# Kernel optimization log

Measured on AMD Instinct MI355X. Metric: run time of the kernel, lower is better.

## Reference

```python
import jax, jax.numpy as jnp
import numpy as np

INPUT_CHANNELS = 1
FIRE_RATE = 0.5
BN_EPS = 1e-5
PAD = 3  # (kernel_size - 1) // 2 for kernel_size=7


def setup_inputs() -> dict:
    key = jax.random.key(0)
    ks = jax.random.split(key, 6)
    B, H, W, C, HID, K = 8, 256, 256, 16, 128, 7
    return {
        "x": jax.random.normal(ks[0], (B, H, W, C), jnp.float32),
        "p0_w": jax.random.normal(ks[1], (K, K, 1, C), jnp.float32) * 0.1,
        "p0_b": jax.random.normal(ks[2], (C,), jnp.float32) * 0.1,
        "fc0_w": jax.random.normal(ks[3], (2 * C, HID), jnp.float32) * (1.0 / np.sqrt(2 * C)),
        "fc0_b": jax.random.normal(ks[4], (HID,), jnp.float32) * 0.1,
        "bn_gamma": jnp.ones((HID,), jnp.float32),
        "bn_beta": jnp.zeros((HID,), jnp.float32),
        "fc1_w": jax.random.normal(ks[5], (HID, C), jnp.float32) * (1.0 / np.sqrt(HID)),
        "steps": 10,
    }


def _depthwise_conv(x, w, b):
    # x: [B,H,W,C], w: [K,K,1,C] depthwise, reflect padding
    xp = jnp.pad(x, ((0, 0), (PAD, PAD), (PAD, PAD), (0, 0)), mode="reflect")
    y = jax.lax.conv_general_dilated(
        xp, w, window_strides=(1, 1), padding="VALID",
        dimension_numbers=("NHWC", "HWIO", "NHWC"),
        feature_group_count=x.shape[-1])
    return y + b


def _step(x, key, p0_w, p0_b, fc0_w, fc0_b, bn_gamma, bn_beta, fc1_w):
    B, H, W, C = x.shape
    # perceive: depthwise conv + identity concat -> [B,H,W,2C]
    y = jnp.concatenate([x, _depthwise_conv(x, p0_w, p0_b)], axis=-1)
    h = y @ fc0_w + fc0_b  # [B,H,W,HID]
    # BatchNorm2d with batch stats over (N, spatial), per hidden channel
    mean = jnp.mean(h, axis=(0, 1, 2), keepdims=True)
    var = jnp.var(h, axis=(0, 1, 2), keepdims=True)
    h = (h - mean) * jax.lax.rsqrt(var + BN_EPS) * bn_gamma + bn_beta
    h = jax.nn.relu(h)
    dx = h @ fc1_w  # [B,H,W,C]
    # stochastic per-cell mask: rand > fire_rate
    mask = (jax.random.uniform(key, (B, H, W, 1)) > FIRE_RATE).astype(dx.dtype)
    x2 = x + dx * mask
    # keep input channels unchanged
    return jnp.concatenate([x[..., :INPUT_CHANNELS], x2[..., INPUT_CHANNELS:]], axis=-1)


def reference(x, p0_w, p0_b, fc0_w, fc0_b, bn_gamma, bn_beta, fc1_w, steps):
    key = jax.random.key(42)
    for s in range(steps):
        x = _step(x, jax.random.fold_in(key, s), p0_w, p0_b, fc0_w, fc0_b,
                  bn_gamma, bn_beta, fc1_w)
    return x
```

## Files before the change

### kernel.cpp

```cpp
#include <hip/hip_runtime.h>
#include <stdint.h>


constexpr int Bn = 8;
constexpr int Hn = 256;
constexpr int Wn = 256;
constexpr int Cn = 16;
constexpr int HIDn = 128;
constexpr int NCELLS = Bn * Hn * Wn;
constexpr int NGRP = 1024;
constexpr int NPAIR = 528;
constexpr int NSTAT = 560;
constexpr int STEPS = 10;

typedef __attribute__((ext_vector_type(8))) short bf16x8;
typedef __attribute__((ext_vector_type(4))) float f32x4;

__host__ __device__ inline uint32_t rotl32(uint32_t v, int r) {
  return (v << r) | (v >> (32 - r));
}

__host__ __device__ inline void tf2x32(uint32_t k0, uint32_t k1,
                                       uint32_t& x0, uint32_t& x1) {
  uint32_t k2 = k0 ^ k1 ^ 0x1BD11BDAu;
  x0 += k0; x1 += k1;
  x0 += x1; x1 = rotl32(x1, 13); x1 ^= x0;
  x0 += x1; x1 = rotl32(x1, 15); x1 ^= x0;
  x0 += x1; x1 = rotl32(x1, 26); x1 ^= x0;
  x0 += x1; x1 = rotl32(x1,  6); x1 ^= x0;
  x0 += k1; x1 += k2 + 1u;
  x0 += x1; x1 = rotl32(x1, 17); x1 ^= x0;
  x0 += x1; x1 = rotl32(x1, 29); x1 ^= x0;
  x0 += x1; x1 = rotl32(x1, 16); x1 ^= x0;
  x0 += x1; x1 = rotl32(x1, 24); x1 ^= x0;
  x0 += k2; x1 += k0 + 2u;
  x0 += x1; x1 = rotl32(x1, 13); x1 ^= x0;
  x0 += x1; x1 = rotl32(x1, 15); x1 ^= x0;
  x0 += x1; x1 = rotl32(x1, 26); x1 ^= x0;
  x0 += x1; x1 = rotl32(x1,  6); x1 ^= x0;
  x0 += k0; x1 += k1 + 3u;
  x0 += x1; x1 = rotl32(x1, 17); x1 ^= x0;
  x0 += x1; x1 = rotl32(x1, 29); x1 ^= x0;
  x0 += x1; x1 = rotl32(x1, 16); x1 ^= x0;
  x0 += x1; x1 = rotl32(x1, 24); x1 ^= x0;
  x0 += k1; x1 += k2 + 4u;
  x0 += x1; x1 = rotl32(x1, 13); x1 ^= x0;
  x0 += x1; x1 = rotl32(x1, 15); x1 ^= x0;
  x0 += x1; x1 = rotl32(x1, 26); x1 ^= x0;
  x0 += x1; x1 = rotl32(x1,  6); x1 ^= x0;
  x0 += k2; x1 += k0 + 5u;
}

__device__ inline float cell_mask(uint32_t fk0, uint32_t fk1, uint32_t ci) {
  uint32_t a = 0u, b2 = ci;
  tf2x32(fk0, fk1, a, b2);
  uint32_t bits = a ^ b2;
  float u = __uint_as_float((bits >> 9) | 0x3f800000u) - 1.0f;
  return (u > 0.5f) ? 1.0f : 0.0f;
}

__device__ inline uint32_t f2bf(float f) {
  uint32_t u = __float_as_uint(f);
  return (u + 0x7fffu + ((u >> 16) & 1u)) >> 16;
}

__global__ __launch_bounds__(256) void nca_prep(const float* __restrict__ fc0w,
                                                const float* __restrict__ fc1w,
                                                uint16_t* __restrict__ w0bf,
                                                uint16_t* __restrict__ w1p) {
  int i = blockIdx.x * 256 + threadIdx.x;
  if (i < 4096) {
    int n = i >> 5, k = i & 31;
    w0bf[i] = (uint16_t)f2bf(fc0w[k * HIDn + n]);
  } else {
    int j = i - 4096;
    int c = j >> 7, kl = j & 127;
    int n = (kl & 7) * 16 + (kl >> 3);
    w1p[j] = (uint16_t)f2bf(fc1w[n * 16 + c]);
  }
}

__global__ __launch_bounds__(256, 4) void nca_convgram(
    const float* __restrict__ x, const float* __restrict__ p0w,
    const float* __restrict__ p0b, uint16_t* __restrict__ ybf,
    float* __restrict__ partials) {
  __shared__ float sW[784];
  __shared__ float sB[16];
  __shared__ __align__(16) short sYT[32 * 256];
  __shared__ float sMom[4 * 32];
  int t = threadIdx.x;
  int lane = t & 63, wid = t >> 6;
  int bid = blockIdx.x;
  int b = bid & 7;
  int rest = bid >> 3;
  int h0 = (rest >> 1) * 4;
  int wbase = (rest & 1) * 128;
  for (int i = t; i < 784; i += 256) sW[i] = p0w[i];
  if (t < 16) sB[t] = p0b[t];
  __syncthreads();

  int wl = t & 127;
  int ch0 = (t >> 7) * 8;
  int w = wbase + wl;
  const float* xb = x + (size_t)b * (Hn * Wn * Cn) + ch0;
  float acc[4][8];
#pragma unroll
  for (int j = 0; j < 4; j++)
#pragma unroll
    for (int c = 0; c < 8; c++) acc[j][c] = 0.0f;

#pragma unroll 1
  for (int r = 0; r < 10; r++) {
    int hi = h0 - 3 + r;
    hi = (hi < 0) ? -hi : ((hi >= Hn) ? (2 * Hn - 2 - hi) : hi);
    const float* xr = xb + (size_t)hi * (Wn * Cn);
#pragma unroll
    for (int dx = 0; dx < 7; dx++) {
      int ww = w + dx - 3;
      ww = (ww < 0) ? -ww : ((ww >= Wn) ? (2 * Wn - 2 - ww) : ww);
      const float4* p = reinterpret_cast<const float4*>(xr + (size_t)ww * Cn);
      float4 v0 = p[0], v1 = p[1];
      float v[8];
      v[0] = v0.x; v[1] = v0.y; v[2] = v0.z; v[3] = v0.w;
      v[4] = v1.x; v[5] = v1.y; v[6] = v1.z; v[7] = v1.w;
#pragma unroll
      for (int j = 0; j < 4; j++) {
        if (r >= j && r <= j + 6) {
          const float* wt = sW + ((r - j) * 7 + dx) * 16 + ch0;
#pragma unroll
          for (int c = 0; c < 8; c++) acc[j][c] += wt[c] * v[c];
        }
      }
    }
  }

  int colc = lane & 15, kg = lane >> 4;
  f32x4 g00 = {0.f, 0.f, 0.f, 0.f}, g01 = g00, g11 = g00, m0 = g00, m1 = g00;
  bf16x8 ones;
#pragma unroll
  for (int e = 0; e < 8; e++) ones[e] = (short)0x3F80;

#pragma unroll
  for (int rr = 0; rr < 2; rr++) {
    if (rr) __syncthreads();
#pragma unroll
    for (int jj = 0; jj < 2; jj++) {
      int j = rr * 2 + jj;
      size_t ci = ((size_t)(b * Hn + h0 + j) * Wn + w);
      int cidx = jj * 128 + wl;
      const float4* pc = reinterpret_cast<const float4*>(
          xb + ((size_t)(h0 + j) * Wn + w) * Cn);
      float4 c0v = pc[0], c1v = pc[1];
      float xcv[8];
      xcv[0] = c0v.x; xcv[1] = c0v.y; xcv[2] = c0v.z; xcv[3] = c0v.w;
      xcv[4] = c1v.x; xcv[5] = c1v.y; xcv[6] = c1v.z; xcv[7] = c1v.w;
      uint32_t pkx[4], pkc[4];
#pragma unroll
      for (int q = 0; q < 4; q++)
        pkx[q] = f2bf(xcv[2 * q]) | (f2bf(xcv[2 * q + 1]) << 16);
#pragma unroll
      for (int q = 0; q < 4; q++)
        pkc[q] = f2bf(acc[j][2 * q] + sB[ch0 + 2 * q]) |
                 (f2bf(acc[j][2 * q + 1] + sB[ch0 + 2 * q + 1]) << 16);
      *reinterpret_cast<uint4*>(ybf + ci * 32 + ch0) =
          make_uint4(pkx[0], pkx[1], pkx[2], pkx[3]);
      *reinterpret_cast<uint4*>(ybf + ci * 32 + 16 + ch0) =
          make_uint4(pkc[0], pkc[1], pkc[2], pkc[3]);
#pragma unroll
      for (int q = 0; q < 4; q++) {
        int cA = ch0 + 2 * q, cB = cA + 1;
        sYT[cA * 256 + (cidx ^ ((cA & 7) << 3))] = (short)(uint16_t)(pkx[q] & 0xffffu);
        sYT[cB * 256 + (cidx ^ ((cB & 7) << 3))] = (short)(uint16_t)(pkx[q] >> 16);
        int cC = 16 + cA, cD = 16 + cB;
        sYT[cC * 256 + (cidx ^ ((cC & 7) << 3))] = (short)(uint16_t)(pkc[q] & 0xffffu);
        sYT[cD * 256 + (cidx ^ ((cD & 7) << 3))] = (short)(uint16_t)(pkc[q] >> 16);
      }
    }
    __syncthreads();
#pragma unroll
    for (int s2 = 0; s2 < 2; s2++) {
      int kbase = wid * 64 + s2 * 32 + kg * 8;
      int chA = colc, chB = 16 + colc;
      bf16x8 f0 = *reinterpret_cast<const bf16x8*>(sYT + chA * 256 + (kbase ^ ((chA & 7) << 3)));
      bf16x8 f1 = *reinterpret_cast<const bf16x8*>(sYT + chB * 256 + (kbase ^ ((chB & 7) << 3)));
      g00 = __builtin_amdgcn_mfma_f32_16x16x32_bf16(f0, f0, g00, 0, 0, 0);
      g01 = __builtin_amdgcn_mfma_f32_16x16x32_bf16(f0, f1, g01, 0, 0, 0);
      g11 = __builtin_amdgcn_mfma_f32_16x16x32_bf16(f1, f1, g11, 0, 0, 0);
      m0  = __builtin_amdgcn_mfma_f32_16x16x32_bf16(f0, ones, m0, 0, 0, 0);
      m1  = __builtin_amdgcn_mfma_f32_16x16x32_bf16(f1, ones, m1, 0, 0, 0);
    }
  }
  if (colc == 0) {
#pragma unroll
    for (int r = 0; r < 4; r++) {
      sMom[wid * 32 + kg * 4 + r] = m0[r];
      sMom[wid * 32 + 16 + kg * 4 + r] = m1[r];
    }
  }
  __syncthreads();
  float* sG = reinterpret_cast<float*>(sYT);
  {
    float* sGw = sG + wid * 1024;
#pragma unroll
    for (int r = 0; r < 4; r++) {
      int rr2 = kg * 4 + r;
      sGw[rr2 * 32 + colc] = g00[r];
      sGw[rr2 * 32 + 16 + colc] = g01[r];
      sGw[(16 + rr2) * 32 + 16 + colc] = g11[r];
    }
  }
  __syncthreads();

  float* outp = partials + (size_t)bid * NSTAT;
  for (int e = t; e < NSTAT; e += 256) {
    float a;
    if (e < NPAIR) {
      int ee = e, i = 0;
      while (ee >= (32 - i)) { ee -= (32 - i); i++; }
      int j = i + ee;
      int gi = i * 32 + j;
      a = sG[gi] + sG[1024 + gi] + sG[2048 + gi] + sG[3072 + gi];
    } else {
      int i = e - NPAIR;
      a = sMom[i] + sMom[32 + i] + sMom[64 + i] + sMom[96 + i];
    }
    outp[e] = a;
  }
}

__global__ __launch_bounds__(256) void nca_reduceA(
    const float* __restrict__ partials, double* __restrict__ sred) {
  __shared__ double red[256];
  int e = blockIdx.x;
  int t = threadIdx.x;
  double acc = 0.0;
  for (int row = t; row < NGRP; row += 256)
    acc += (double)partials[(size_t)row * NSTAT + e];
  red[t] = acc;
  __syncthreads();
  for (int s2 = 128; s2 > 0; s2 >>= 1) {
    if (t < s2) red[t] += red[t + s2];
    __syncthreads();
  }
  if (t == 0) sred[e] = red[0];
}

__global__ __launch_bounds__(128) void nca_reduceB(
    const double* __restrict__ sred, const float* __restrict__ fc0w,
    const float* __restrict__ gamma, const float* __restrict__ beta,
    float* __restrict__ ss) {
  __shared__ double S[NSTAT];
  int t = threadIdx.x;
  for (int i = t; i < NSTAT; i += 128) S[i] = sred[i];
  __syncthreads();
  double wv[32];
#pragma unroll
  for (int k = 0; k < 32; k++) wv[k] = (double)fc0w[k * HIDn + t];
  double mean_g = 0.0, q = 0.0;
  int e = 0;
  for (int i = 0; i < 32; i++) {
    mean_g += wv[i] * S[NPAIR + i];
    q += wv[i] * wv[i] * S[e]; e++;
    for (int j = i + 1; j < 32; j++) { q += 2.0 * wv[i] * wv[j] * S[e]; e++; }
  }
  const double invN = 1.0 / (double)NCELLS;
  mean_g *= invN; q *= invN;
  double var = q - mean_g * mean_g;
  double scale = (double)gamma[t] / sqrt(var + 1e-5);
  ss[2 * t]     = (float)scale;
  ss[2 * t + 1] = (float)((double)beta[t] - mean_g * scale);
}

__global__ __launch_bounds__(256) void nca_update_mfma(
    const float* __restrict__ x, const uint16_t* __restrict__ ybf,
    const uint16_t* __restrict__ w0bf, const uint16_t* __restrict__ w1p,
    const float* __restrict__ ssg, float* __restrict__ xout,
    uint32_t fk0, uint32_t fk1) {
  __shared__ short hbuf[4][16 * 128];
  int t = threadIdx.x;
  int lane = t & 63, wid = t >> 6;
  int col = lane & 15, g = lane >> 4;
  short* hb = hbuf[wid];

  bf16x8 b0[8];
#pragma unroll
  for (int nt = 0; nt < 8; nt++) {
    int n = nt * 16 + col;
    b0[nt] = *reinterpret_cast<const bf16x8*>(w0bf + n * 32 + g * 8);
  }
  bf16x8 b2[4];
#pragma unroll
  for (int kk = 0; kk < 4; kk++)
    b2[kk] = *reinterpret_cast<const bf16x8*>(w1p + col * 128 + kk * 32 + g * 8);
  float sc[8], sh[8];
#pragma unroll
  for (int nt = 0; nt < 8; nt++) {
    float2 v = reinterpret_cast<const float2*>(ssg)[nt * 16 + col];
    sc[nt] = v.x; sh[nt] = v.y;
  }

  uint32_t waveBase = (uint32_t)blockIdx.x * 1024u + (uint32_t)wid * 256u;
  for (int grp = 0; grp < 4; grp++) {
    uint32_t grpBase = waveBase + (uint32_t)grp * 64u;
    float mval = cell_mask(fk0, fk1, grpBase + (uint32_t)lane);
#pragma unroll 1
    for (int tt = 0; tt < 4; tt++) {
      uint32_t tb = grpBase + (uint32_t)tt * 16u;
      bf16x8 a0 = *reinterpret_cast<const bf16x8*>(
          ybf + (size_t)(tb + col) * 32 + g * 8);
      float xv[4];
#pragma unroll
      for (int r = 0; r < 4; r++)
        xv[r] = x[(size_t)(tb + g * 4 + r) * Cn + col];
      f32x4 h[8];
#pragma unroll
      for (int nt = 0; nt < 8; nt++) {
        f32x4 z = {0.f, 0.f, 0.f, 0.f};
        h[nt] = __builtin_amdgcn_mfma_f32_16x16x32_bf16(a0, b0[nt], z, 0, 0, 0);
      }
#pragma unroll
      for (int r = 0; r < 4; r++) {
        int m = g * 4 + r;
        uint32_t u[4];
#pragma unroll
        for (int q = 0; q < 4; q++) {
          float v0 = fmaxf(h[2 * q][r] * sc[2 * q] + sh[2 * q], 0.0f);
          float v1 = fmaxf(h[2 * q + 1][r] * sc[2 * q + 1] + sh[2 * q + 1], 0.0f);
          u[q] = f2bf(v0) | (f2bf(v1) << 16);
        }
        int idx = m * 128 + ((col * 8) ^ ((m & 7) << 3));
        *reinterpret_cast<uint4*>(hb + idx) = make_uint4(u[0], u[1], u[2], u[3]);
      }
      f32x4 dx = {0.f, 0.f, 0.f, 0.f};
#pragma unroll
      for (int kk = 0; kk < 4; kk++) {
        int idx = col * 128 + (((kk * 32) + g * 8) ^ ((col & 7) << 3));
        bf16x8 a2 = *reinterpret_cast<const bf16x8*>(hb + idx);
        dx = __builtin_amdgcn_mfma_f32_16x16x32_bf16(a2, b2[kk], dx, 0, 0, 0);
      }
#pragma unroll
      for (int r = 0; r < 4; r++) {
        int m = g * 4 + r;
        float mk = __shfl(mval, tt * 16 + m);
        float o = xv[r] + dx[r] * mk;
        if (col == 0) o = xv[r];
        xout[(size_t)(tb + m) * Cn + col] = o;
      }
    }
  }
}

extern "C" void kernel_launch(void* const* d_in, const int* in_sizes, int n_in,
                              void* d_out, int out_size, void* d_ws, size_t ws_size,
                              hipStream_t stream) {
  (void)in_sizes; (void)n_in; (void)out_size; (void)ws_size;
  const float* x0    = (const float*)d_in[0];
  const float* p0w   = (const float*)d_in[1];
  const float* p0b   = (const float*)d_in[2];
  const float* fc0w  = (const float*)d_in[3];
  const float* gamma = (const float*)d_in[5];
  const float* beta  = (const float*)d_in[6];
  const float* fc1w  = (const float*)d_in[7];

  size_t off = 0;
  float* ws_x = (float*)((char*)d_ws + off); off += (size_t)NCELLS * Cn * 4;
  uint16_t* ws_ybf = (uint16_t*)((char*)d_ws + off); off += (size_t)NCELLS * 32 * 2;
  float* ws_part = (float*)((char*)d_ws + off); off += (size_t)NGRP * NSTAT * 4;
  double* ws_sred = (double*)((char*)d_ws + off); off += (size_t)NSTAT * 8;
  float* ws_ss = (float*)((char*)d_ws + off); off += (size_t)HIDn * 2 * 4;
  uint16_t* ws_w0bf = (uint16_t*)((char*)d_ws + off); off += 4096 * 2;
  uint16_t* ws_w1p = (uint16_t*)((char*)d_ws + off); off += 2048 * 2;
  float* out = (float*)d_out;

  nca_prep<<<24, 256, 0, stream>>>(fc0w, fc1w, ws_w0bf, ws_w1p);

  const float* xin = x0;
  for (int s = 0; s < STEPS; s++) {
    uint32_t fk0 = 0u, fk1 = (uint32_t)s;
    tf2x32(0u, 42u, fk0, fk1);
    float* xo = (((STEPS - 1 - s) & 1) != 0) ? ws_x : out;

    nca_convgram<<<NGRP, 256, 0, stream>>>(xin, p0w, p0b, ws_ybf, ws_part);
    nca_reduceA<<<NSTAT, 256, 0, stream>>>(ws_part, ws_sred);
    nca_reduceB<<<1, 128, 0, stream>>>(ws_sred, fc0w, gamma, beta, ws_ss);
    nca_update_mfma<<<NCELLS / 1024, 256, 0, stream>>>(xin, ws_ybf, ws_w0bf,
                                                       ws_w1p, ws_ss, xo, fk0, fk1);
    xin = xo;
  }
}
```

Baseline: 873.5 us.

## Stage conv rows in double-buffered LDS, vectorize stat reduction, halve update work per block

The depthwise conv kernel now loads each input row once cooperatively into a double-buffered, XOR-swizzled shared-memory tile, prefetching the next row while computing the current one, instead of each thread reading seven overlapping global float4 pairs. The stats reduction kernel handles four statistics per block with float4 loads, cutting the block count by four. The update kernel processes 512 cells per block rather than 1024, doubling the grid for more parallelism. These changes add LDS pressure and a per-row barrier, which could lower occupancy in the conv kernel.

```diff
diff --git a/kernel.cpp b/kernel.cpp
--- a/kernel.cpp
+++ b/kernel.cpp
@@ -12,6 +12,7 @@
 constexpr int NPAIR = 528;
 constexpr int NSTAT = 560;
 constexpr int STEPS = 10;
+constexpr int RCELLS = 134;
 
 typedef __attribute__((ext_vector_type(8))) short bf16x8;
 typedef __attribute__((ext_vector_type(4))) float f32x4;
@@ -80,12 +81,17 @@
   }
 }
 
+__device__ inline int row_fi(int c, int q) {
+  return (((c << 6) + (q << 4)) ^ ((c & 7) << 4)) >> 2;
+}
+
 __global__ __launch_bounds__(256, 4) void nca_convgram(
     const float* __restrict__ x, const float* __restrict__ p0w,
     const float* __restrict__ p0b, uint16_t* __restrict__ ybf,
     float* __restrict__ partials) {
   __shared__ float sW[784];
   __shared__ float sB[16];
+  __shared__ __align__(16) float sRow[2][RCELLS * 16];
   __shared__ __align__(16) short sYT[32 * 256];
   __shared__ float sMom[4 * 32];
   int t = threadIdx.x;
@@ -97,12 +103,39 @@
   int wbase = (rest & 1) * 128;
   for (int i = t; i < 784; i += 256) sW[i] = p0w[i];
   if (t < 16) sB[t] = p0b[t];
+
+  int wl = t & 127;
+  int half = t >> 7;
+  int ch0 = half * 8;
+  int w = wbase + wl;
+  const float* xb = x + (size_t)b * (Hn * Wn * Cn);
+
+  auto rowptr = [&](int r) -> const float* {
+    int hi = h0 - 3 + r;
+    hi = (hi < 0) ? -hi : ((hi >= Hn) ? (2 * Hn - 2 - hi) : hi);
+    return xb + (size_t)hi * (Wn * Cn);
+  };
+  auto ld16 = [&](const float* xr, int i) -> float4 {
+    int c = i >> 2, q = i & 3;
+    int wc = wbase - 3 + c;
+    wc = (wc < 0) ? -wc : ((wc >= Wn) ? (2 * Wn - 2 - wc) : wc);
+    return *reinterpret_cast<const float4*>(xr + (size_t)wc * Cn + q * 4);
+  };
+
+  {
+    const float* xr = rowptr(0);
+    float4 p0 = ld16(xr, t);
+    float4 p1 = ld16(xr, t + 256);
+    float4 p2;
+    if (t < 536 - 512) p2 = ld16(xr, t + 512);
+    float* rb = sRow[0];
+    *reinterpret_cast<float4*>(rb + row_fi(t >> 2, t & 3)) = p0;
+    *reinterpret_cast<float4*>(rb + row_fi((t + 256) >> 2, t & 3)) = p1;
+    if (t < 536 - 512)
+      *reinterpret_cast<float4*>(rb + row_fi((t + 512) >> 2, t & 3)) = p2;
+  }
   __syncthreads();
 
-  int wl = t & 127;
-  int ch0 = (t >> 7) * 8;
-  int w = wbase + wl;
-  const float* xb = x + (size_t)b * (Hn * Wn * Cn) + ch0;
   float acc[4][8];
 #pragma unroll
   for (int j = 0; j < 4; j++)
@@ -111,27 +144,40 @@
 
 #pragma unroll 1
   for (int r = 0; r < 10; r++) {
-    int hi = h0 - 3 + r;
-    hi = (hi < 0) ? -hi : ((hi >= Hn) ? (2 * Hn - 2 - hi) : hi);
-    const float* xr = xb + (size_t)hi * (Wn * Cn);
+    int cur = r & 1;
+    float4 p0, p1, p2;
+    if (r < 9) {
+      const float* xr = rowptr(r + 1);
+      p0 = ld16(xr, t);
+      p1 = ld16(xr, t + 256);
+      if (t < 536 - 512) p2 = ld16(xr, t + 512);
+    }
+    const float* rb = sRow[cur];
 #pragma unroll
     for (int dx = 0; dx < 7; dx++) {
-      int ww = w + dx - 3;
-      ww = (ww < 0) ? -ww : ((ww >= Wn) ? (2 * Wn - 2 - ww) : ww);
-      const float4* p = reinterpret_cast<const float4*>(xr + (size_t)ww * Cn);
-      float4 v0 = p[0], v1 = p[1];
+      int c = wl + dx;
+      float4 va = *reinterpret_cast<const float4*>(rb + row_fi(c, 2 * half));
+      float4 vb = *reinterpret_cast<const float4*>(rb + row_fi(c, 2 * half + 1));
       float v[8];
-      v[0] = v0.x; v[1] = v0.y; v[2] = v0.z; v[3] = v0.w;
-      v[4] = v1.x; v[5] = v1.y; v[6] = v1.z; v[7] = v1.w;
+      v[0] = va.x; v[1] = va.y; v[2] = va.z; v[3] = va.w;
+      v[4] = vb.x; v[5] = vb.y; v[6] = vb.z; v[7] = vb.w;
 #pragma unroll
       for (int j = 0; j < 4; j++) {
         if (r >= j && r <= j + 6) {
           const float* wt = sW + ((r - j) * 7 + dx) * 16 + ch0;
 #pragma unroll
-          for (int c = 0; c < 8; c++) acc[j][c] += wt[c] * v[c];
+          for (int c2 = 0; c2 < 8; c2++) acc[j][c2] += wt[c2] * v[c2];
         }
       }
     }
+    if (r < 9) {
+      float* wb2 = sRow[cur ^ 1];
+      *reinterpret_cast<float4*>(wb2 + row_fi(t >> 2, t & 3)) = p0;
+      *reinterpret_cast<float4*>(wb2 + row_fi((t + 256) >> 2, t & 3)) = p1;
+      if (t < 536 - 512)
+        *reinterpret_cast<float4*>(wb2 + row_fi((t + 512) >> 2, t & 3)) = p2;
+    }
+    __syncthreads();
   }
 
   int colc = lane & 15, kg = lane >> 4;
@@ -149,7 +195,7 @@
       size_t ci = ((size_t)(b * Hn + h0 + j) * Wn + w);
       int cidx = jj * 128 + wl;
       const float4* pc = reinterpret_cast<const float4*>(
-          xb + ((size_t)(h0 + j) * Wn + w) * Cn);
+          xb + ((size_t)(h0 + j) * Wn + w) * Cn + ch0);
       float4 c0v = pc[0], c1v = pc[1];
       float xcv[8];
       xcv[0] = c0v.x; xcv[1] = c0v.y; xcv[2] = c0v.z; xcv[3] = c0v.w;
@@ -230,19 +276,24 @@
 
 __global__ __launch_bounds__(256) void nca_reduceA(
     const float* __restrict__ partials, double* __restrict__ sred) {
-  __shared__ double red[256];
-  int e = blockIdx.x;
+  __shared__ double red[256][4];
+  int e4 = blockIdx.x * 4;
   int t = threadIdx.x;
-  double acc = 0.0;
-  for (int row = t; row < NGRP; row += 256)
-    acc += (double)partials[(size_t)row * NSTAT + e];
-  red[t] = acc;
+  double a0 = 0.0, a1 = 0.0, a2 = 0.0, a3 = 0.0;
+  for (int row = t; row < NGRP; row += 256) {
+    float4 v = *reinterpret_cast<const float4*>(partials + (size_t)row * NSTAT + e4);
+    a0 += v.x; a1 += v.y; a2 += v.z; a3 += v.w;
+  }
+  red[t][0] = a0; red[t][1] = a1; red[t][2] = a2; red[t][3] = a3;
   __syncthreads();
   for (int s2 = 128; s2 > 0; s2 >>= 1) {
-    if (t < s2) red[t] += red[t + s2];
+    if (t < s2) {
+#pragma unroll
+      for (int q = 0; q < 4; q++) red[t][q] += red[t + s2][q];
+    }
     __syncthreads();
   }
-  if (t == 0) sred[e] = red[0];
+  if (t < 4) sred[e4 + t] = red[0][t];
 }
 
 __global__ __launch_bounds__(128) void nca_reduceB(
@@ -299,8 +350,8 @@
     sc[nt] = v.x; sh[nt] = v.y;
   }
 
-  uint32_t waveBase = (uint32_t)blockIdx.x * 1024u + (uint32_t)wid * 256u;
-  for (int grp = 0; grp < 4; grp++) {
+  uint32_t waveBase = (uint32_t)blockIdx.x * 512u + (uint32_t)wid * 128u;
+  for (int grp = 0; grp < 2; grp++) {
     uint32_t grpBase = waveBase + (uint32_t)grp * 64u;
     float mval = cell_mask(fk0, fk1, grpBase + (uint32_t)lane);
 #pragma unroll 1
@@ -381,10 +432,10 @@
     float* xo = (((STEPS - 1 - s) & 1) != 0) ? ws_x : out;
 
     nca_convgram<<<NGRP, 256, 0, stream>>>(xin, p0w, p0b, ws_ybf, ws_part);
-    nca_reduceA<<<NSTAT, 256, 0, stream>>>(ws_part, ws_sred);
+    nca_reduceA<<<140, 256, 0, stream>>>(ws_part, ws_sred);
     nca_reduceB<<<1, 128, 0, stream>>>(ws_sred, fc0w, gamma, beta, ws_ss);
-    nca_update_mfma<<<NCELLS / 1024, 256, 0, stream>>>(xin, ws_ybf, ws_w0bf,
-                                                       ws_w1p, ws_ss, xo, fk0, fk1);
+    nca_update_mfma<<<NCELLS / 512, 256, 0, stream>>>(xin, ws_ybf, ws_w0bf,
+                                                      ws_w1p, ws_ss, xo, fk0, fk1);
     xin = xo;
   }
 }
```

Measured after the change: 804.1 us. 1.09x faster.
